# Kernel tuning notes

Measured on AMD Instinct MI355X. Metric: run time of the kernel, lower is better.

The kernel has to match this reference:

```python
import jax, jax.numpy as jnp
import numpy as np

L, D, H, S, V, B = 8, 512, 8, 64, 66, 256
DH = D // H
EPS = 1e-10  # module's LayerNorm eps, added to std (not var)


def layernorm(x, g, b):
    # torch.std_mean default: unbiased std (ddof=1)
    mean = jnp.mean(x, axis=-1, keepdims=True)
    std = jnp.std(x, axis=-1, ddof=1, keepdims=True)
    return (x - mean) / (std + EPS) * g + b


def setup_inputs() -> dict:
    key = jax.random.key(0)
    ks = iter(jax.random.split(key, 32))
    def n(shape, scale=0.02):
        return jax.random.normal(next(ks), shape, dtype=jnp.float32) * scale
    return {
        "input_ids": jax.random.randint(next(ks), (B, S), 0, V),
        "targets": jax.random.randint(next(ks), (B, S), 0, V),
        "tok_emb": n((V, D), 1.0),
        "pos_emb": n((S, D), 1.0),
        "Wq": n((L, D, H, DH)), "Wk": n((L, D, H, DH)), "Wv": n((L, D, H, DH)),
        "Wo": n((L, D, D)), "bo": jnp.zeros((L, D), jnp.float32),
        "W1": n((L, D, 4 * D)), "b1": jnp.zeros((L, 4 * D), jnp.float32),
        "W2": n((L, 4 * D, D)), "b2": jnp.zeros((L, D), jnp.float32),
        "ln1_g": jnp.ones((L, D), jnp.float32), "ln1_b": jnp.zeros((L, D), jnp.float32),
        "ln2_g": jnp.ones((L, D), jnp.float32), "ln2_b": jnp.zeros((L, D), jnp.float32),
        "lnf_g": jnp.ones((D,), jnp.float32), "lnf_b": jnp.zeros((D,), jnp.float32),
        "Wu": n((D, V)), "bu": jnp.zeros((V,), jnp.float32),
    }


def reference(input_ids, targets, tok_emb, pos_emb, Wq, Wk, Wv, Wo, bo,
              W1, b1, W2, b2, ln1_g, ln1_b, ln2_g, ln2_b, lnf_g, lnf_b, Wu, bu):
    x = tok_emb[input_ids] + pos_emb[None, :, :]  # [B,S,D]
    scale = 1.0 / jnp.sqrt(jnp.float32(D))        # module scales by 1/sqrt(d_model)
    mask = jnp.tril(jnp.ones((S, S), dtype=bool))
    for l in range(L):
        h = layernorm(x, ln1_g[l], ln1_b[l])
        q = jnp.einsum('bsd,dhe->bhse', h, Wq[l])
        k = jnp.einsum('bsd,dhe->bhse', h, Wk[l])
        v = jnp.einsum('bsd,dhe->bhse', h, Wv[l])
        scores = jnp.einsum('bhse,bhte->bhst', q, k) * scale
        scores = jnp.where(mask, scores, -jnp.inf)
        attn = jax.nn.softmax(scores, axis=-1)
        o = jnp.einsum('bhst,bhte->bhse', attn, v)
        o = o.transpose(0, 2, 1, 3).reshape(B, S, D)  # concat heads (head order preserved)
        x = x + o @ Wo[l] + bo[l]
        h2 = layernorm(x, ln2_g[l], ln2_b[l])
        hid = jax.nn.gelu(h2 @ W1[l] + b1[l], approximate=False)  # nn.GELU exact
        x = x + hid @ W2[l] + b2[l]
    x = layernorm(x, lnf_g, lnf_b)
    logits = x @ Wu + bu  # [B,S,V]
    logp = jax.nn.log_softmax(logits, axis=-1)
    loss = -jnp.mean(jnp.take_along_axis(logp, targets[..., None], axis=-1))
    return logits, loss
```

## Files before the change

kernel.cpp:

```cpp
#include <hip/hip_runtime.h>
#include <hip/hip_bf16.h>
#include <math.h>

#define D_MODEL 512
#define NHEAD   8
#define DHEAD   64
#define SEQ     64
#define BATCH   256
#define NLAYER  8
#define VOCAB   66
#define FFDIM   2048
#define NTOK    (BATCH * SEQ)

typedef __attribute__((ext_vector_type(8))) short short8;
typedef __attribute__((ext_vector_type(4))) float f32x4;
typedef __attribute__((ext_vector_type(16))) float f32x16;

__device__ inline void async_copy16(const void* g, void* l) {
    __builtin_amdgcn_global_load_lds(
        (const __attribute__((address_space(1))) void*)g,
        (__attribute__((address_space(3))) void*)l,
        16, 0, 0);
}

__global__ __launch_bounds__(256) void transpose_conv(
        const float* __restrict__ W, __hip_bfloat16* __restrict__ Wt,
        int K, int M, size_t inLS, size_t outLS, int rowOff) {
    __shared__ float tile[32][33];
    int m0 = blockIdx.x * 32, k0 = blockIdx.y * 32;
    const float* Wl = W + blockIdx.z * inLS;
    __hip_bfloat16* Wtl = Wt + blockIdx.z * outLS;
    int t = threadIdx.x;
    #pragma unroll
    for (int p = 0; p < 4; p++) {
        int idx = t + p * 256;
        int kr = idx >> 5, mc = idx & 31;
        tile[kr][mc] = Wl[(size_t)(k0 + kr) * M + m0 + mc];
    }
    __syncthreads();
    #pragma unroll
    for (int p = 0; p < 4; p++) {
        int idx = t + p * 256;
        int mr = idx >> 5, kc = idx & 31;
        Wtl[(size_t)(rowOff + m0 + mr) * K + k0 + kc] = __float2bfloat16(tile[kc][mr]);
    }
}

__global__ __launch_bounds__(256) void conv_wu(
        const float* __restrict__ Wu, __hip_bfloat16* __restrict__ WuT) {
    int idx = blockIdx.x * 256 + threadIdx.x;
    int m = idx >> 9, k = idx & 511;
    WuT[idx] = __float2bfloat16(m < VOCAB ? Wu[(size_t)k * VOCAB + m] : 0.f);
}

__global__ void embed_kernel(const int* __restrict__ ids, const float* __restrict__ tok,
                             const float* __restrict__ pos, float* __restrict__ x) {
    int idx = blockIdx.x * 256 + threadIdx.x;
    int n = idx >> 9;
    int d = idx & 511;
    int s = n & (SEQ - 1);
    x[idx] = tok[ids[n] * D_MODEL + d] + pos[s * D_MODEL + d];
}

__global__ __launch_bounds__(256) void ln_kernel(
        const float* __restrict__ x, const float* __restrict__ g,
        const float* __restrict__ b, __hip_bfloat16* __restrict__ y) {
    int row = blockIdx.x * 4 + (threadIdx.x >> 6);
    int lane = threadIdx.x & 63;
    const float* xr = x + (size_t)row * D_MODEL + lane * 8;
    f32x4 v0 = *(const f32x4*)xr;
    f32x4 v1 = *(const f32x4*)(xr + 4);
    float s = 0.f, ss = 0.f;
    #pragma unroll
    for (int e = 0; e < 4; e++) { s += v0[e] + v1[e]; ss += v0[e] * v0[e] + v1[e] * v1[e]; }
    #pragma unroll
    for (int o = 1; o < 64; o <<= 1) {
        s  += __shfl_xor(s, o);
        ss += __shfl_xor(ss, o);
    }
    float mean = s / (float)D_MODEL;
    float var = (ss - (float)D_MODEL * mean * mean) / (float)(D_MODEL - 1);
    float denom = sqrtf(fmaxf(var, 0.f)) + 1e-10f;
    f32x4 g0 = *(const f32x4*)(g + lane * 8);
    f32x4 g1 = *(const f32x4*)(g + lane * 8 + 4);
    f32x4 b0 = *(const f32x4*)(b + lane * 8);
    f32x4 b1 = *(const f32x4*)(b + lane * 8 + 4);
    short8 outv;
    #pragma unroll
    for (int e = 0; e < 4; e++) {
        outv[e]     = ((__hip_bfloat16_raw)__float2bfloat16((v0[e] - mean) / denom * g0[e] + b0[e])).x;
        outv[e + 4] = ((__hip_bfloat16_raw)__float2bfloat16((v1[e] - mean) / denom * g1[e] + b1[e])).x;
    }
    *(short8*)((short*)y + (size_t)row * D_MODEL + lane * 8) = outv;
}

template <int ACT, int OUTMODE>
__global__ __launch_bounds__(256) void mfma_gemm(
        const __hip_bfloat16* __restrict__ A, const __hip_bfloat16* __restrict__ Bt,
        const float* __restrict__ bias, const float* addsrc,
        void* Cout, int K, int M, int ldc, int mstore) {
    __shared__ __align__(16) short As[128 * 32];
    __shared__ __align__(16) short Bs[128 * 32];
    int tid = threadIdx.x;
    int lane = tid & 63, wave = tid >> 6;
    int row0 = blockIdx.y * 128, col0 = blockIdx.x * 128;
    int wr = (wave >> 1) * 64, wc = (wave & 1) * 64;
    int l31 = lane & 31, h32 = lane >> 5;

    f32x16 acc[2][2] = {};

    int sr = tid >> 2;
    int scol = (tid & 3) * 8;
    const short* Ag = (const short*)A + (size_t)(row0 + sr) * K + scol;
    const short* Bg = (const short*)Bt + (size_t)(col0 + sr) * K + scol;
    short* Al = As + sr * 32 + scol;
    short* Bl = Bs + sr * 32 + scol;

    for (int k0 = 0; k0 < K; k0 += 32) {
        async_copy16(Ag + k0, Al);
        async_copy16(Ag + (size_t)64 * K + k0, Al + 64 * 32);
        async_copy16(Bg + k0, Bl);
        async_copy16(Bg + (size_t)64 * K + k0, Bl + 64 * 32);
        __syncthreads();
        short8 af[2][2], bf[2][2];
        #pragma unroll
        for (int i = 0; i < 2; i++)
            #pragma unroll
            for (int kh = 0; kh < 2; kh++) {
                af[i][kh] = *(const short8*)(As + (wr + i * 32 + l31) * 32 + kh * 16 + h32 * 8);
                bf[i][kh] = *(const short8*)(Bs + (wc + i * 32 + l31) * 32 + kh * 16 + h32 * 8);
            }
        #pragma unroll
        for (int i = 0; i < 2; i++)
            #pragma unroll
            for (int j = 0; j < 2; j++) {
                acc[i][j] = __builtin_amdgcn_mfma_f32_32x32x16_bf16(af[i][0], bf[j][0], acc[i][j], 0, 0, 0);
                acc[i][j] = __builtin_amdgcn_mfma_f32_32x32x16_bf16(af[i][1], bf[j][1], acc[i][j], 0, 0, 0);
            }
        __syncthreads();
    }

    #pragma unroll
    for (int j = 0; j < 2; j++) {
        int col = col0 + wc + j * 32 + l31;
        if (OUTMODE == 2 && col >= mstore) continue;
        float bv = bias ? bias[col] : 0.f;
        #pragma unroll
        for (int i = 0; i < 2; i++) {
            int rbase = row0 + wr + i * 32 + 4 * h32;
            #pragma unroll
            for (int r = 0; r < 16; r++) {
                int row = rbase + (r & 3) + 8 * (r >> 2);
                float v = acc[i][j][r] + bv;
                if (OUTMODE == 1) v += addsrc[(size_t)row * M + col];
                if (ACT == 1) v = 0.5f * v * (1.f + erff(v * 0.70710678118654752f));
                if (OUTMODE == 0)
                    ((__hip_bfloat16*)Cout)[(size_t)row * M + col] = __float2bfloat16(v);
                else
                    ((float*)Cout)[(size_t)row * ldc + col] = v;
            }
        }
    }
}

#define PSTRIDE 72
__global__ __launch_bounds__(256) void attn_mfma(
        const __hip_bfloat16* __restrict__ QKV, __hip_bfloat16* __restrict__ O) {
    __shared__ __align__(16) short Vt[64 * PSTRIDE];
    __shared__ __align__(16) short P[64 * PSTRIDE];
    int bh = blockIdx.x;
    int b = bh >> 3, h = bh & 7;
    int t = threadIdx.x;
    int lane = t & 63, wave = t >> 6;
    int l15 = lane & 15, quad = lane >> 4;
    const float scale = 0.04419417382415922f;
    const short* base = (const short*)QKV + (size_t)(b * SEQ) * 1536 + h * DHEAD;

    {
        int j0 = (t >> 3) * 2;
        int c0 = (t & 7) * 8;
        const short* vrow = base + 1024 + (size_t)j0 * 1536 + c0;
        short8 va = *(const short8*)vrow;
        short8 vb = *(const short8*)(vrow + 1536);
        #pragma unroll
        for (int s = 0; s < 8; s++) {
            unsigned int packed = ((unsigned int)(unsigned short)vb[s] << 16) |
                                  (unsigned int)(unsigned short)va[s];
            *(unsigned int*)&Vt[(c0 + s) * PSTRIDE + j0] = packed;
        }
    }

    int r0 = wave * 16;
    short8 aq[2], bk[4][2];
    #pragma unroll
    for (int k = 0; k < 2; k++)
        aq[k] = *(const short8*)(base + (size_t)(r0 + l15) * 1536 + quad * 8 + 32 * k);
    #pragma unroll
    for (int j = 0; j < 4; j++)
        #pragma unroll
        for (int k = 0; k < 2; k++)
            bk[j][k] = *(const short8*)(base + 512 + (size_t)(j * 16 + l15) * 1536 + quad * 8 + 32 * k);

    f32x4 sc[4];
    #pragma unroll
    for (int j = 0; j < 4; j++) {
        f32x4 z = {};
        z = __builtin_amdgcn_mfma_f32_16x16x32_bf16(aq[0], bk[j][0], z, 0, 0, 0);
        sc[j] = __builtin_amdgcn_mfma_f32_16x16x32_bf16(aq[1], bk[j][1], z, 0, 0, 0);
    }

    float p[4][4];
    #pragma unroll
    for (int reg = 0; reg < 4; reg++) {
        int r = r0 + quad * 4 + reg;
        float m = -INFINITY;
        #pragma unroll
        for (int j = 0; j < 4; j++) {
            int c = j * 16 + l15;
            float s = (c <= r) ? sc[j][reg] * scale : -INFINITY;
            p[j][reg] = s;
            m = fmaxf(m, s);
        }
        #pragma unroll
        for (int o = 1; o < 16; o <<= 1) m = fmaxf(m, __shfl_xor(m, o));
        float sum = 0.f;
        #pragma unroll
        for (int j = 0; j < 4; j++) {
            float e = (p[j][reg] == -INFINITY) ? 0.f : expf(p[j][reg] - m);
            p[j][reg] = e;
            sum += e;
        }
        #pragma unroll
        for (int o = 1; o < 16; o <<= 1) sum += __shfl_xor(sum, o);
        float inv = 1.f / sum;
        #pragma unroll
        for (int j = 0; j < 4; j++) p[j][reg] *= inv;
    }

    #pragma unroll
    for (int j = 0; j < 4; j++)
        #pragma unroll
        for (int reg = 0; reg < 4; reg++) {
            int r = r0 + quad * 4 + reg;
            P[r * PSTRIDE + j * 16 + l15] =
                ((__hip_bfloat16_raw)__float2bfloat16(p[j][reg])).x;
        }

    __syncthreads();

    short8 ap[2];
    #pragma unroll
    for (int k = 0; k < 2; k++)
        ap[k] = *(const short8*)(P + (r0 + l15) * PSTRIDE + quad * 8 + 32 * k);
    #pragma unroll
    for (int jt = 0; jt < 4; jt++) {
        short8 bv0 = *(const short8*)(Vt + (jt * 16 + l15) * PSTRIDE + quad * 8);
        short8 bv1 = *(const short8*)(Vt + (jt * 16 + l15) * PSTRIDE + quad * 8 + 32);
        f32x4 o = {};
        o = __builtin_amdgcn_mfma_f32_16x16x32_bf16(ap[0], bv0, o, 0, 0, 0);
        o = __builtin_amdgcn_mfma_f32_16x16x32_bf16(ap[1], bv1, o, 0, 0, 0);
        #pragma unroll
        for (int reg = 0; reg < 4; reg++) {
            int r = r0 + quad * 4 + reg;
            int c = jt * 16 + l15;
            O[(size_t)(b * SEQ + r) * D_MODEL + h * DHEAD + c] = __float2bfloat16(o[reg]);
        }
    }
}

__global__ void zero_kernel(float* p) { if (threadIdx.x == 0) *p = 0.f; }

__global__ __launch_bounds__(256) void loss_kernel(
        const float* __restrict__ lg, const int* __restrict__ tgt,
        float* __restrict__ loss) {
    int wave = threadIdx.x >> 6;
    int l = threadIdx.x & 63;
    float local = 0.f;
    for (int row = blockIdx.x * 4 + wave; row < NTOK; row += gridDim.x * 4) {
        const float* lr = lg + (size_t)row * VOCAB;
        float a = lr[l];
        float bx = (l < VOCAB - 64) ? lr[64 + l] : -INFINITY;
        float m = fmaxf(a, bx);
        #pragma unroll
        for (int o = 32; o >= 1; o >>= 1) m = fmaxf(m, __shfl_xor(m, o));
        float s = expf(a - m) + ((l < VOCAB - 64) ? expf(bx - m) : 0.f);
        #pragma unroll
        for (int o = 32; o >= 1; o >>= 1) s += __shfl_xor(s, o);
        if (l == 0) local += lr[tgt[row]] - m - logf(s);
    }
    if (l == 0) atomicAdd(loss, -local / (float)NTOK);
}

extern "C" void kernel_launch(void* const* d_in, const int* in_sizes, int n_in,
                              void* d_out, int out_size, void* d_ws, size_t ws_size,
                              hipStream_t stream) {
    const int*   input_ids = (const int*)  d_in[0];
    const int*   targets   = (const int*)  d_in[1];
    const float* tok_emb   = (const float*)d_in[2];
    const float* pos_emb   = (const float*)d_in[3];
    const float* Wq        = (const float*)d_in[4];
    const float* Wk        = (const float*)d_in[5];
    const float* Wv        = (const float*)d_in[6];
    const float* Wo        = (const float*)d_in[7];
    const float* bo        = (const float*)d_in[8];
    const float* W1        = (const float*)d_in[9];
    const float* b1        = (const float*)d_in[10];
    const float* W2        = (const float*)d_in[11];
    const float* b2        = (const float*)d_in[12];
    const float* ln1_g     = (const float*)d_in[13];
    const float* ln1_b     = (const float*)d_in[14];
    const float* ln2_g     = (const float*)d_in[15];
    const float* ln2_b     = (const float*)d_in[16];
    const float* lnf_g     = (const float*)d_in[17];
    const float* lnf_b     = (const float*)d_in[18];
    const float* Wu        = (const float*)d_in[19];
    const float* bu        = (const float*)d_in[20];

    float* out  = (float*)d_out;
    float* loss = out + (size_t)NTOK * VOCAB;

    const size_t ND = (size_t)NTOK * D_MODEL;
    float* x             = (float*)d_ws;
    __hip_bfloat16* h    = (__hip_bfloat16*)(x + ND);
    __hip_bfloat16* qkv  = h + ND;
    __hip_bfloat16* ob   = qkv + 3 * ND;
    __hip_bfloat16* hid  = qkv;
    __hip_bfloat16* wqkvT = ob + ND;
    __hip_bfloat16* woT   = wqkvT + (size_t)NLAYER * 1536 * 512;
    __hip_bfloat16* w1T   = woT + (size_t)NLAYER * 512 * 512;
    __hip_bfloat16* w2T   = w1T + (size_t)NLAYER * 2048 * 512;
    __hip_bfloat16* wuT   = w2T + (size_t)NLAYER * 2048 * 512;

    transpose_conv<<<dim3(16, 16, NLAYER), 256, 0, stream>>>(Wq, wqkvT, 512, 512,
        (size_t)512 * 512, (size_t)1536 * 512, 0);
    transpose_conv<<<dim3(16, 16, NLAYER), 256, 0, stream>>>(Wk, wqkvT, 512, 512,
        (size_t)512 * 512, (size_t)1536 * 512, 512);
    transpose_conv<<<dim3(16, 16, NLAYER), 256, 0, stream>>>(Wv, wqkvT, 512, 512,
        (size_t)512 * 512, (size_t)1536 * 512, 1024);
    transpose_conv<<<dim3(16, 16, NLAYER), 256, 0, stream>>>(Wo, woT, 512, 512,
        (size_t)512 * 512, (size_t)512 * 512, 0);
    transpose_conv<<<dim3(64, 16, NLAYER), 256, 0, stream>>>(W1, w1T, 512, 2048,
        (size_t)512 * 2048, (size_t)2048 * 512, 0);
    transpose_conv<<<dim3(16, 64, NLAYER), 256, 0, stream>>>(W2, w2T, 2048, 512,
        (size_t)2048 * 512, (size_t)512 * 2048, 0);
    conv_wu<<<(128 * 512) / 256, 256, 0, stream>>>(Wu, wuT);

    embed_kernel<<<(NTOK * D_MODEL) / 256, 256, 0, stream>>>(input_ids, tok_emb, pos_emb, x);

    for (int l = 0; l < NLAYER; l++) {
        ln_kernel<<<NTOK / 4, 256, 0, stream>>>(x, ln1_g + l * D_MODEL, ln1_b + l * D_MODEL, h);
        mfma_gemm<0, 0><<<dim3(12, 128), 256, 0, stream>>>(
            h, wqkvT + (size_t)l * 1536 * 512, nullptr, nullptr, qkv, 512, 1536, 1536, 1536);
        attn_mfma<<<BATCH * NHEAD, 256, 0, stream>>>(qkv, ob);
        mfma_gemm<0, 1><<<dim3(4, 128), 256, 0, stream>>>(
            ob, woT + (size_t)l * 512 * 512, bo + l * D_MODEL, x, x, 512, 512, 512, 512);
        ln_kernel<<<NTOK / 4, 256, 0, stream>>>(x, ln2_g + l * D_MODEL, ln2_b + l * D_MODEL, h);
        mfma_gemm<1, 0><<<dim3(16, 128), 256, 0, stream>>>(
            h, w1T + (size_t)l * 2048 * 512, b1 + l * FFDIM, nullptr, hid, 512, 2048, 2048, 2048);
        mfma_gemm<0, 1><<<dim3(4, 128), 256, 0, stream>>>(
            hid, w2T + (size_t)l * 2048 * 512, b2 + l * D_MODEL, x, x, 2048, 512, 512, 512);
    }

    ln_kernel<<<NTOK / 4, 256, 0, stream>>>(x, lnf_g, lnf_b, h);
    mfma_gemm<0, 2><<<dim3(1, 128), 256, 0, stream>>>(
        h, wuT, bu, nullptr, out, 512, 128, VOCAB, VOCAB);
    zero_kernel<<<1, 64, 0, stream>>>(loss);
    loss_kernel<<<128, 256, 0, stream>>>(out, targets, loss);
}
```

Measured before the change: 2.395 ms.

## Double GEMM K-tile to 64 and XOR-swizzle LDS layout

The MFMA GEMM now stages a 64-wide K slice per iteration instead of 32, which halves the number of barrier pairs per tile. Each 16-byte chunk's column within a row is XOR-swizzled by the row index so fragment reads from LDS avoid bank conflicts. This doubles LDS use per block and raises register pressure from holding more fragments. The global-to-LDS copies are still not double-buffered.

Result: faster. 2.115 ms (-11.7%).

```diff
diff --git a/kernel.cpp b/kernel.cpp
--- a/kernel.cpp
+++ b/kernel.cpp
@@ -99,44 +99,53 @@
         const __hip_bfloat16* __restrict__ A, const __hip_bfloat16* __restrict__ Bt,
         const float* __restrict__ bias, const float* addsrc,
         void* Cout, int K, int M, int ldc, int mstore) {
-    __shared__ __align__(16) short As[128 * 32];
-    __shared__ __align__(16) short Bs[128 * 32];
+    __shared__ __align__(16) short As[128 * 64];
+    __shared__ __align__(16) short Bs[128 * 64];
     int tid = threadIdx.x;
     int lane = tid & 63, wave = tid >> 6;
     int row0 = blockIdx.y * 128, col0 = blockIdx.x * 128;
     int wr = (wave >> 1) * 64, wc = (wave & 1) * 64;
     int l31 = lane & 31, h32 = lane >> 5;
+    int l7 = l31 & 7;
 
     f32x16 acc[2][2] = {};
 
-    int sr = tid >> 2;
-    int scol = (tid & 3) * 8;
-    const short* Ag = (const short*)A + (size_t)(row0 + sr) * K + scol;
-    const short* Bg = (const short*)Bt + (size_t)(col0 + sr) * K + scol;
-    short* Al = As + sr * 32 + scol;
-    short* Bl = Bs + sr * 32 + scol;
-
-    for (int k0 = 0; k0 < K; k0 += 32) {
-        async_copy16(Ag + k0, Al);
-        async_copy16(Ag + (size_t)64 * K + k0, Al + 64 * 32);
-        async_copy16(Bg + k0, Bl);
-        async_copy16(Bg + (size_t)64 * K + k0, Bl + 64 * 32);
+    int srow[4], skg[4];
+    #pragma unroll
+    for (int s = 0; s < 4; s++) {
+        int u = s * 256 + tid;
+        srow[s] = u >> 3;
+        skg[s] = (u & 7) ^ (srow[s] & 7);
+    }
+
+    for (int k0 = 0; k0 < K; k0 += 64) {
+        #pragma unroll
+        for (int s = 0; s < 4; s++) {
+            int u = s * 256 + tid;
+            async_copy16((const short*)A + (size_t)(row0 + srow[s]) * K + k0 + skg[s] * 8,
+                         As + u * 8);
+            async_copy16((const short*)Bt + (size_t)(col0 + srow[s]) * K + k0 + skg[s] * 8,
+                         Bs + u * 8);
+        }
         __syncthreads();
-        short8 af[2][2], bf[2][2];
+        short8 af[2][4], bf[2][4];
         #pragma unroll
         for (int i = 0; i < 2; i++)
             #pragma unroll
-            for (int kh = 0; kh < 2; kh++) {
-                af[i][kh] = *(const short8*)(As + (wr + i * 32 + l31) * 32 + kh * 16 + h32 * 8);
-                bf[i][kh] = *(const short8*)(Bs + (wc + i * 32 + l31) * 32 + kh * 16 + h32 * 8);
+            for (int kk = 0; kk < 4; kk++) {
+                int kg = kk * 2 + h32;
+                int c = kg ^ l7;
+                af[i][kk] = *(const short8*)(As + ((wr + i * 32 + l31) * 8 + c) * 8);
+                bf[i][kk] = *(const short8*)(Bs + ((wc + i * 32 + l31) * 8 + c) * 8);
             }
         #pragma unroll
         for (int i = 0; i < 2; i++)
             #pragma unroll
-            for (int j = 0; j < 2; j++) {
-                acc[i][j] = __builtin_amdgcn_mfma_f32_32x32x16_bf16(af[i][0], bf[j][0], acc[i][j], 0, 0, 0);
-                acc[i][j] = __builtin_amdgcn_mfma_f32_32x32x16_bf16(af[i][1], bf[j][1], acc[i][j], 0, 0, 0);
-            }
+            for (int j = 0; j < 2; j++)
+                #pragma unroll
+                for (int kk = 0; kk < 4; kk++)
+                    acc[i][j] = __builtin_amdgcn_mfma_f32_32x32x16_bf16(
+                        af[i][kk], bf[j][kk], acc[i][j], 0, 0, 0);
         __syncthreads();
     }
 
```
